# Optimization experiments

Measured on AMD Instinct MI355X. Metric: run time of the kernel, lower is better.

## Reference

```python
import jax, jax.numpy as jnp
import numpy as np

B, PLEN, QLEN, D = 16, 1024, 256, 256
MASK_VALUE = -10000000.0


def setup_inputs() -> dict:
    key = jax.random.key(0)
    k1, k2, k3 = jax.random.split(key, 3)
    passage = jax.random.normal(k1, (B, PLEN, D), dtype=jnp.float32)
    question = jax.random.normal(k2, (B, QLEN, D), dtype=jnp.float32)
    passage_mask = (jnp.arange(PLEN)[None, :] >= int(PLEN * 0.9)).astype(jnp.int32)
    passage_mask = jnp.broadcast_to(passage_mask, (B, PLEN))
    question_mask = (jnp.arange(QLEN)[None, :] >= int(QLEN * 0.9)).astype(jnp.int32)
    question_mask = jnp.broadcast_to(question_mask, (B, QLEN))
    # score_linear: Linear(3d, 1) -> weight vector [3d], scalar bias
    W = jax.random.normal(k3, (3 * D,), dtype=jnp.float32) * 0.05
    b = jnp.zeros((1,), dtype=jnp.float32)
    return {"passage": passage, "question": question,
            "passage_mask": passage_mask, "question_mask": question_mask,
            "W": W, "b": b}


def reference(passage, question, passage_mask, question_mask, W, b):
    d = passage.shape[-1]
    # Decompose Linear([p, q, p*q]) @ W + b into three additive terms --
    # identical math to concat+linear, no [b,plen,qlen,3d] intermediate.
    w_p, w_q, w_pq = W[:d], W[d:2 * d], W[2 * d:]
    score = (jnp.einsum('bpd,d->bp', passage, w_p)[:, :, None]
             + jnp.einsum('bqd,d->bq', question, w_q)[:, None, :]
             + jnp.einsum('bpd,bqd->bpq', passage * w_pq, question)
             + b[0])  # [b, plen, qlen]
    pm = passage_mask.astype(score.dtype)
    qm = question_mask.astype(score.dtype)
    keep = (1.0 - pm)[:, :, None] * (1.0 - qm)[:, None, :]  # [b,plen,qlen]
    mask = 1.0 - keep
    score = score * keep + mask * MASK_VALUE
    p2q_weights = jax.nn.softmax(score, axis=2)
    q2p_weights = jax.nn.softmax(jnp.transpose(score, (0, 2, 1)), axis=2)
    p2q_weights = p2q_weights * keep
    q2p_weights = q2p_weights * jnp.transpose(keep, (0, 2, 1))
    p2q_attention = jnp.einsum('bpq,bqd->bpd', p2q_weights, question)
    q2p_attention = jnp.einsum('bqp,bpd->bqd', q2p_weights, passage)
    coattention = jnp.einsum('bpq,bqd->bpd', p2q_weights, q2p_attention)
    return (p2q_attention, coattention)
```

## Files before the change

kernel.cpp:

```cpp
#include <hip/hip_runtime.h>
#include <math.h>

#define NB 16
#define PLEN 1024
#define QLEN 256
#define DIM 256
#define MASKV -10000000.0f

typedef __attribute__((ext_vector_type(8))) short short8;
typedef __attribute__((ext_vector_type(4))) float f32x4;

union u4x16 { unsigned short u[4]; int2 v; };
union u8x16 { unsigned short u[8]; int4 v; };
union u16x16 { unsigned short u[16]; int4 v[2]; };

__device__ inline unsigned short f2bf(float x) {
  unsigned int u = __float_as_uint(x);
  u += 0x7FFF + ((u >> 16) & 1);
  return (unsigned short)(u >> 16);
}
__device__ inline float bf2f(unsigned short u) {
  return __uint_as_float(((unsigned int)u) << 16);
}
__device__ inline int4 pack8(float4 a, float4 b) {
  u8x16 o;
  o.u[0] = f2bf(a.x); o.u[1] = f2bf(a.y); o.u[2] = f2bf(a.z); o.u[3] = f2bf(a.w);
  o.u[4] = f2bf(b.x); o.u[5] = f2bf(b.y); o.u[6] = f2bf(b.z); o.u[7] = f2bf(b.w);
  return o.v;
}

__global__ __launch_bounds__(1024) void k_scoreA(
    const float* __restrict__ passage, const float* __restrict__ question,
    const float* __restrict__ Wg,
    const int* __restrict__ pmask, const int* __restrict__ qmask,
    const float* __restrict__ bias,
    unsigned short* __restrict__ PbT, unsigned short* __restrict__ QbT,
    float* __restrict__ CL, float* __restrict__ RS,
    unsigned short* __restrict__ P2Q, unsigned short* __restrict__ P2Qt) {
  int bid0 = blockIdx.x;
  int bid = (bid0 & 7) * 32 + (bid0 >> 3);
  int b = bid >> 4;
  int tile = bid & 15;
  int p0 = tile * 64;
  int t = threadIdx.x, lane = t & 63, wv = t >> 6;
  int s = wv >> 2, h = wv & 3;
  __shared__ __align__(16) unsigned short As[2][64][40];
  __shared__ __align__(16) unsigned short Bs[2][256][40];
  __shared__ __align__(16) unsigned short Pl[64][264];
  __shared__ float redL[4][256];
  __shared__ float rowL[64][4];
  __shared__ float spS[64];
  __shared__ float sqS[256];

  int rb = t >> 2, cb = (t & 3) * 8;
  int pr = t >> 4, pc = (t & 15) * 2;
  const float* psrc = passage + ((size_t)b * PLEN + p0 + pr) * DIM;
  const float* qsrc = question + ((size_t)b * QLEN + rb) * DIM;
  const float* wq = Wg + DIM;

  f32x4 acc[4] = {};
  float spp = 0.f, sqq = 0.f;
  float4 qa = *(const float4*)&qsrc[cb];
  float4 qb_ = *(const float4*)&qsrc[cb + 4];
  float2 xv = *(const float2*)(psrc + pc);
  {
    sqq += qa.x * wq[cb]     + qa.y * wq[cb + 1] + qa.z * wq[cb + 2] + qa.w * wq[cb + 3]
         + qb_.x * wq[cb + 4] + qb_.y * wq[cb + 5] + qb_.z * wq[cb + 6] + qb_.w * wq[cb + 7];
    *(int4*)&Bs[0][rb][cb] = pack8(qa, qb_);
    spp += xv.x * Wg[pc] + xv.y * Wg[pc + 1];
    unsigned int raw = (unsigned int)f2bf(xv.x) | (((unsigned int)f2bf(xv.y)) << 16);
    unsigned int wgt = (unsigned int)f2bf(xv.x * Wg[2 * DIM + pc])
                     | (((unsigned int)f2bf(xv.y * Wg[2 * DIM + pc + 1])) << 16);
    *(unsigned int*)&Pl[pr][pc] = raw;
    *(unsigned int*)&As[0][pr][pc] = wgt;
  }
  __syncthreads();
  int cur = 0;
  for (int ki = 0; ki < 8; ++ki) {
    float2 xn; float4 qa2, qb2;
    if (ki < 7) {
      int kt = (ki + 1) * 32;
      qa2 = *(const float4*)&qsrc[kt + cb];
      qb2 = *(const float4*)&qsrc[kt + cb + 4];
      xn = *(const float2*)(psrc + kt + pc);
    }
    short8 af = *(const short8*)&As[cur][s * 16 + (lane & 15)][(lane >> 4) * 8];
    for (int j = 0; j < 4; ++j) {
      short8 bf = *(const short8*)&Bs[cur][h * 64 + j * 16 + (lane & 15)][(lane >> 4) * 8];
      acc[j] = __builtin_amdgcn_mfma_f32_16x16x32_bf16(af, bf, acc[j], 0, 0, 0);
    }
    if (ki < 7) {
      int kt = (ki + 1) * 32;
      int dq = kt + cb, dp = kt + pc;
      sqq += qa2.x * wq[dq]     + qa2.y * wq[dq + 1] + qa2.z * wq[dq + 2] + qa2.w * wq[dq + 3]
           + qb2.x * wq[dq + 4] + qb2.y * wq[dq + 5] + qb2.z * wq[dq + 6] + qb2.w * wq[dq + 7];
      spp += xn.x * Wg[dp] + xn.y * Wg[dp + 1];
      unsigned int raw = (unsigned int)f2bf(xn.x) | (((unsigned int)f2bf(xn.y)) << 16);
      unsigned int wgt = (unsigned int)f2bf(xn.x * Wg[2 * DIM + dp])
                       | (((unsigned int)f2bf(xn.y * Wg[2 * DIM + dp + 1])) << 16);
      int nxt = cur ^ 1;
      *(unsigned int*)&Pl[pr][dp] = raw;
      *(unsigned int*)&As[nxt][pr][pc] = wgt;
      *(int4*)&Bs[nxt][rb][cb] = pack8(qa2, qb2);
      cur = nxt;
    }
    __syncthreads();
  }

  sqq += __shfl_xor(sqq, 1, 64);
  sqq += __shfl_xor(sqq, 2, 64);
  if ((t & 3) == 0) sqS[rb] = sqq;
  spp += __shfl_xor(spp, 1, 64);
  spp += __shfl_xor(spp, 2, 64);
  spp += __shfl_xor(spp, 4, 64);
  spp += __shfl_xor(spp, 8, 64);
  if ((t & 15) == 0) spS[pr] = spp;
  {
    int d = t >> 2, ch = t & 3;
    u16x16 o;
    for (int e = 0; e < 16; ++e) o.u[e] = Pl[ch * 16 + e][d];
    unsigned short* dst = PbT + ((size_t)b * DIM + d) * PLEN + p0 + ch * 16;
    *(int4*)dst = o.v[0];
    *(int4*)(dst + 8) = o.v[1];
  }
  __syncthreads();

  float b0 = bias[0];
  float spv[4]; int pmv[4];
  for (int r = 0; r < 4; ++r) {
    int rl = s * 16 + (lane >> 4) * 4 + r;
    spv[r] = spS[rl] + b0;
    pmv[r] = pmask[b * PLEN + p0 + rl];
  }
  float sqv[4]; int qmv[4];
  for (int j = 0; j < 4; ++j) {
    int q = h * 64 + j * 16 + (lane & 15);
    sqv[j] = sqS[q];
    qmv[j] = qmask[b * QLEN + q];
  }
  for (int j = 0; j < 4; ++j)
    for (int r = 0; r < 4; ++r) {
      float v = acc[j][r] + spv[r] + sqv[j];
      acc[j][r] = (pmv[r] | qmv[j]) ? 0.0f : __expf(v);
    }

  for (int j = 0; j < 4; ++j) {
    float e = acc[j][0] + acc[j][1] + acc[j][2] + acc[j][3];
    e += __shfl_xor(e, 16, 64);
    e += __shfl_xor(e, 32, 64);
    if ((lane >> 4) == 0)
      redL[s][h * 64 + j * 16 + (lane & 15)] = e;
  }
  for (int r = 0; r < 4; ++r) {
    int rl = s * 16 + (lane >> 4) * 4 + r;
    float l = acc[0][r] + acc[1][r] + acc[2][r] + acc[3][r];
    for (int msk = 1; msk <= 8; msk <<= 1) l += __shfl_xor(l, msk, 64);
    if ((lane & 15) == 0) rowL[rl][h] = l;
  }
  __syncthreads();

  if (t < 256) {
    int q = t;
    CL[((size_t)b * 16 + tile) * QLEN + q] = redL[0][q] + redL[1][q] + redL[2][q] + redL[3][q];
  }

  for (int r = 0; r < 4; ++r) {
    int rl = s * 16 + (lane >> 4) * 4 + r;
    float l = rowL[rl][0] + rowL[rl][1] + rowL[rl][2] + rowL[rl][3];
    if (h == 0 && (lane & 15) == 0)
      RS[(size_t)b * PLEN + p0 + rl] = l;
    float inv = (l > 0.f) ? 1.0f / l : 0.0f;
    for (int j = 0; j < 4; ++j)
      Pl[rl][h * 64 + j * 16 + (lane & 15)] = f2bf(acc[j][r] * inv);
  }
  __syncthreads();

  for (int k = 0; k < 2; ++k) {
    int idx = t + k * 1024;
    int row = idx >> 5, c8 = idx & 31;
    *(int4*)&P2Q[((size_t)b * PLEN + p0 + row) * QLEN + c8 * 8] = *(const int4*)&Pl[row][c8 * 8];
  }
  {
    int q = t >> 2, pcc = t & 3;
    u16x16 o;
    for (int e = 0; e < 16; ++e) o.u[e] = Pl[pcc * 16 + e][q];
    unsigned short* dst = P2Qt + ((size_t)b * QLEN + q) * PLEN + p0 + pcc * 16;
    *(int4*)dst = o.v[0];
    *(int4*)(dst + 8) = o.v[1];
  }

  if (tile < 4) {
    __syncthreads();
    int r0 = tile * 64;
    const float* src = question + ((size_t)b * QLEN + r0) * DIM;
    int row = t >> 4, c0 = (t & 15) * 16;
    for (int i = 0; i < 4; ++i) {
      int d = c0 + i * 4;
      float4 x = *(const float4*)&src[(size_t)row * DIM + d];
      u4x16 tv;
      tv.u[0] = f2bf(x.x); tv.u[1] = f2bf(x.y); tv.u[2] = f2bf(x.z); tv.u[3] = f2bf(x.w);
      *(int2*)&Pl[row][d] = tv.v;
    }
    __syncthreads();
    for (int it = 0; it < 2; ++it) {
      int g = t + it * 1024;
      int d = g >> 3, ch = g & 7;
      u8x16 o;
      for (int e = 0; e < 8; ++e) o.u[e] = Pl[ch * 8 + e][d];
      *(int4*)&QbT[(size_t)(b * DIM + d) * QLEN + r0 + ch * 8] = o.v;
    }
  }
}

__global__ __launch_bounds__(512) void k_mid(
    const unsigned short* __restrict__ P2Qt, const unsigned short* __restrict__ PbT,
    const unsigned short* __restrict__ P2Q, const unsigned short* __restrict__ QbT,
    const float* __restrict__ RS, const float* __restrict__ CL,
    unsigned short* __restrict__ QATTt, float* __restrict__ out1) {
  __shared__ __align__(16) char smem[40960];
  int t = threadIdx.x, lane = t & 63, wid = t >> 6;

  if (blockIdx.x < NB * 16) {
    int bid = blockIdx.x;
    int b = bid >> 4, dt = (bid >> 2) & 3, qt = bid & 3;
    int wm = wid >> 2, wn = wid & 3;
    typedef unsigned short row72[72];
    row72* Wt = (row72*)smem;
    row72* At = (row72*)(smem + 18432);
    float* CSs = (float*)(smem + 36864);
    if (t < 64) {
      int q = qt * 64 + t;
      float L = 0.f;
      for (int tm = 0; tm < 16; ++tm)
        L += CL[((size_t)b * 16 + tm) * QLEN + q];
      CSs[t] = (L > 0.f) ? 1.0f / L : 0.0f;
    }

    int rrow = t >> 3;
    int pch = (t & 7) * 8;
    const unsigned short* Wsrc = P2Qt + ((size_t)b * QLEN + qt * 64 + rrow) * PLEN + pch;
    const unsigned short* Asrc = PbT + ((size_t)b * DIM + dt * 64 + rrow) * PLEN + pch;
    const float* rsB = RS + (size_t)b * PLEN + pch;

    f32x4 acc[2] = {};
    int4 wvv = *(const int4*)Wsrc;
    int4 av = *(const int4*)Asrc;
    float4 rs0 = *(const float4*)rsB, rs1 = *(const float4*)(rsB + 4);
    __syncthreads();
    float cs = CSs[rrow];

    {
      float rsv[8] = {rs0.x, rs0.y, rs0.z, rs0.w, rs1.x, rs1.y, rs1.z, rs1.w};
      const unsigned short* wu = (const unsigned short*)&wvv;
      u8x16 wo;
#pragma unroll
      for (int e = 0; e < 8; ++e) wo.u[e] = f2bf(bf2f(wu[e]) * rsv[e] * cs);
      *(int4*)&Wt[rrow][pch] = wo.v;
      *(int4*)&At[rrow][pch] = av;
    }
    __syncthreads();
    int cur = 0;
    for (int ps = 0; ps < 16; ++ps) {
      if (ps < 15) {
        int off = (ps + 1) * 64;
        wvv = *(const int4*)(Wsrc + off);
        av = *(const int4*)(Asrc + off);
        rs0 = *(const float4*)(rsB + off); rs1 = *(const float4*)(rsB + off + 4);
      }
      for (int kk = 0; kk < 64; kk += 32) {
        short8 bf = *(const short8*)&Wt[cur * 64 + wn * 16 + (lane & 15)][kk + (lane >> 4) * 8];
        for (int i = 0; i < 2; ++i) {
          short8 af = *(const short8*)&At[cur * 64 + wm * 32 + i * 16 + (lane & 15)][kk + (lane >> 4) * 8];
          acc[i] = __builtin_amdgcn_mfma_f32_16x16x32_bf16(af, bf, acc[i], 0, 0, 0);
        }
      }
      if (ps < 15) {
        float rsv[8] = {rs0.x, rs0.y, rs0.z, rs0.w, rs1.x, rs1.y, rs1.z, rs1.w};
        const unsigned short* wu = (const unsigned short*)&wvv;
        u8x16 wo;
#pragma unroll
        for (int e = 0; e < 8; ++e) wo.u[e] = f2bf(bf2f(wu[e]) * rsv[e] * cs);
        int nxt = cur ^ 1;
        *(int4*)&Wt[nxt * 64 + rrow][pch] = wo.v;
        *(int4*)&At[nxt * 64 + rrow][pch] = av;
        cur = nxt;
      }
      __syncthreads();
    }
    int d0 = dt * 64 + wm * 32, q0 = qt * 64 + wn * 16;
    for (int i = 0; i < 2; ++i)
      for (int rr = 0; rr < 4; ++rr) {
        int d = d0 + i * 16 + (lane >> 4) * 4 + rr;
        QATTt[((size_t)b * DIM + d) * QLEN + q0 + (lane & 15)] = f2bf(acc[i][rr]);
      }
  } else {
    int u = blockIdx.x - NB * 16;
    int b = u >> 5, tm = (u >> 1) & 15, tn = u & 1;
    const unsigned short* A  = P2Q + ((size_t)b * PLEN + tm * 64) * QLEN;
    const unsigned short* B1 = QbT + ((size_t)b * DIM + tn * 128) * QLEN;
    typedef unsigned short row40[40];
    row40* As2 = (row40*)smem;
    row40* Bq = (row40*)(smem + 10240);
    int wm = wid >> 2, wn = wid & 3;
    f32x4 acc1[2][2] = {};
    int r = t >> 2, c = (t & 3) * 8;
    int4 rb1 = *(const int4*)&B1[(size_t)r * QLEN + c];
    int4 rav;
    if (t < 256) rav = *(const int4*)&A[(size_t)r * QLEN + c];
    *(int4*)&Bq[r][c] = rb1;
    if (t < 256) *(int4*)&As2[r][c] = rav;
    __syncthreads();
    int cur = 0;
    for (int ki = 0; ki < 8; ++ki) {
      if (ki < 7) {
        int kt = (ki + 1) * 32;
        rb1 = *(const int4*)&B1[(size_t)r * QLEN + kt + c];
        if (t < 256) rav = *(const int4*)&A[(size_t)r * QLEN + kt + c];
      }
      short8 af[2], b1v[2];
      for (int i = 0; i < 2; ++i)
        af[i] = *(const short8*)&As2[cur * 64 + wm * 32 + i * 16 + (lane & 15)][(lane >> 4) * 8];
      for (int j = 0; j < 2; ++j)
        b1v[j] = *(const short8*)&Bq[cur * 128 + wn * 32 + j * 16 + (lane & 15)][(lane >> 4) * 8];
      for (int i = 0; i < 2; ++i)
        for (int j = 0; j < 2; ++j)
          acc1[i][j] = __builtin_amdgcn_mfma_f32_16x16x32_bf16(af[i], b1v[j], acc1[i][j], 0, 0, 0);
      if (ki < 7) {
        int nxt = cur ^ 1;
        *(int4*)&Bq[nxt * 128 + r][c] = rb1;
        if (t < 256) *(int4*)&As2[nxt * 64 + r][c] = rav;
        cur = nxt;
      }
      __syncthreads();
    }
    int p0 = tm * 64 + wm * 32, d0 = tn * 128 + wn * 32;
    for (int i = 0; i < 2; ++i)
      for (int rr = 0; rr < 4; ++rr) {
        int p = p0 + i * 16 + (lane >> 4) * 4 + rr;
        size_t rowo = ((size_t)b * PLEN + p) * DIM;
        for (int j = 0; j < 2; ++j) {
          int d = d0 + j * 16 + (lane & 15);
          out1[rowo + d] = acc1[i][j][rr];
        }
      }
  }
}

__global__ __launch_bounds__(512) void k_final2(
    const unsigned short* __restrict__ P2Q, const unsigned short* __restrict__ QATTt,
    float* __restrict__ out2) {
  int bid = blockIdx.x;
  int b = bid >> 5, tm = (bid >> 1) & 15, tn = bid & 1;
  const unsigned short* A  = P2Q + ((size_t)b * PLEN + tm * 64) * QLEN;
  const unsigned short* B2 = QATTt + ((size_t)b * DIM + tn * 128) * QLEN;
  __shared__ __align__(16) unsigned short As[2][64][40];
  __shared__ __align__(16) unsigned short Bc[2][128][40];
  int t = threadIdx.x, lane = t & 63, wid = t >> 6;
  int wm = wid >> 2, wn = wid & 3;
  f32x4 acc[2][2] = {};
  int r = t >> 2, c = (t & 3) * 8;
  int4 rb2 = *(const int4*)&B2[(size_t)r * QLEN + c];
  int4 rav;
  if (t < 256) rav = *(const int4*)&A[(size_t)r * QLEN + c];
  *(int4*)&Bc[0][r][c] = rb2;
  if (t < 256) *(int4*)&As[0][r][c] = rav;
  __syncthreads();
  int cur = 0;
  for (int ki = 0; ki < 8; ++ki) {
    if (ki < 7) {
      int kt = (ki + 1) * 32;
      rb2 = *(const int4*)&B2[(size_t)r * QLEN + kt + c];
      if (t < 256) rav = *(const int4*)&A[(size_t)r * QLEN + kt + c];
    }
    short8 af[2], bc[2];
    for (int i = 0; i < 2; ++i)
      af[i] = *(const short8*)&As[cur][wm * 32 + i * 16 + (lane & 15)][(lane >> 4) * 8];
    for (int j = 0; j < 2; ++j)
      bc[j] = *(const short8*)&Bc[cur][wn * 32 + j * 16 + (lane & 15)][(lane >> 4) * 8];
    for (int i = 0; i < 2; ++i)
      for (int j = 0; j < 2; ++j)
        acc[i][j] = __builtin_amdgcn_mfma_f32_16x16x32_bf16(af[i], bc[j], acc[i][j], 0, 0, 0);
    if (ki < 7) {
      int nxt = cur ^ 1;
      *(int4*)&Bc[nxt][r][c] = rb2;
      if (t < 256) *(int4*)&As[nxt][r][c] = rav;
      cur = nxt;
    }
    __syncthreads();
  }
  int p0 = tm * 64 + wm * 32, d0 = tn * 128 + wn * 32;
  for (int i = 0; i < 2; ++i)
    for (int rr = 0; rr < 4; ++rr) {
      int p = p0 + i * 16 + (lane >> 4) * 4 + rr;
      size_t rowo = ((size_t)b * PLEN + p) * DIM;
      for (int j = 0; j < 2; ++j) {
        int d = d0 + j * 16 + (lane & 15);
        out2[rowo + d] = acc[i][j][rr];
      }
    }
}

extern "C" void kernel_launch(void* const* d_in, const int* in_sizes, int n_in,
                              void* d_out, int out_size, void* d_ws, size_t ws_size,
                              hipStream_t stream) {
  const float* passage  = (const float*)d_in[0];
  const float* question = (const float*)d_in[1];
  const int*   pmask    = (const int*)d_in[2];
  const int*   qmask    = (const int*)d_in[3];
  const float* W        = (const float*)d_in[4];
  const float* bias     = (const float*)d_in[5];
  float* out = (float*)d_out;

  const size_t NS = (size_t)NB * PLEN * QLEN;
  const size_t NQ = (size_t)NB * QLEN * DIM;
  char* w = (char*)d_ws;
  unsigned short* PbT  = (unsigned short*)w; w += NS * 2;
  unsigned short* QbT  = (unsigned short*)w; w += NQ * 2;
  unsigned short* P2Q  = (unsigned short*)w; w += NS * 2;
  unsigned short* P2Qt = (unsigned short*)w; w += NS * 2;
  unsigned short* QATTt = (unsigned short*)w; w += NQ * 2;
  float* CL = (float*)w;                     w += (size_t)NB * 16 * QLEN * 4;
  float* RS = (float*)w;

  float* out1 = out;
  float* out2 = out + (size_t)NB * PLEN * DIM;

  k_scoreA<<<dim3(NB * 16), dim3(1024), 0, stream>>>(
      passage, question, W, pmask, qmask, bias, PbT, QbT, CL, RS, P2Q, P2Qt);
  k_mid<<<dim3(NB * 48), dim3(512), 0, stream>>>(
      P2Qt, PbT, P2Q, QbT, RS, CL, QATTt, out1);
  k_final2<<<dim3(NB * 32), dim3(512), 0, stream>>>(
      P2Q, QATTt, out2);
}
```

Measured before the change: 53.58 us.

## Split score kernel over query halves and defer row normalization to consumers

The score kernel now launches 512 blocks of 512 threads, each covering a 64x128 score tile instead of 64x256, which doubles the grid and shrinks LDS use so more blocks can be resident. The blocks store unnormalized exponentials plus per-half row sums. The 1/rowsum scaling moves into the epilogues of the p2q and coattention GEMMs, which drops the per-element rowsum multiply in k_mid's q2p weighting. The passage bf16 transpose is reassigned to the qh==0 blocks. The cost is some extra stored partial sums and redundant inverse computation in the downstream kernels.

Result: faster. 51.99 us (-3.0%).

```diff
diff --git a/kernel.cpp b/kernel.cpp
--- a/kernel.cpp
+++ b/kernel.cpp
@@ -29,64 +29,80 @@
   return o.v;
 }
 
-__global__ __launch_bounds__(1024) void k_scoreA(
+typedef unsigned short row40[40];
+typedef unsigned short row136[136];
+typedef unsigned short row264[264];
+
+#define SM_AS   0
+#define SM_BS   10240
+#define SM_REDL 30720
+#define SM_ROWL 32768
+#define SM_SPS  33280
+#define SM_SQS  33536
+#define SM_PL   34048
+#define SM_TOT  51456
+
+__global__ __launch_bounds__(512, 4) void k_scoreA(
     const float* __restrict__ passage, const float* __restrict__ question,
     const float* __restrict__ Wg,
     const int* __restrict__ pmask, const int* __restrict__ qmask,
     const float* __restrict__ bias,
     unsigned short* __restrict__ PbT, unsigned short* __restrict__ QbT,
-    float* __restrict__ CL, float* __restrict__ RS,
-    unsigned short* __restrict__ P2Q, unsigned short* __restrict__ P2Qt) {
+    float* __restrict__ CL, float* __restrict__ RS2,
+    unsigned short* __restrict__ E, unsigned short* __restrict__ Et) {
+  __shared__ __align__(16) char smem[SM_TOT];
+  row40* As = (row40*)(smem + SM_AS);
+  row40* Bs = (row40*)(smem + SM_BS);
+  float (*redL)[128] = (float(*)[128])(smem + SM_REDL);
+  float (*rowL)[2] = (float(*)[2])(smem + SM_ROWL);
+  float* spS = (float*)(smem + SM_SPS);
+  float* sqS = (float*)(smem + SM_SQS);
+  row136* Pl = (row136*)(smem + SM_PL);
+
   int bid0 = blockIdx.x;
-  int bid = (bid0 & 7) * 32 + (bid0 >> 3);
-  int b = bid >> 4;
-  int tile = bid & 15;
-  int p0 = tile * 64;
+  int bid = (bid0 & 7) * 64 + (bid0 >> 3);
+  int b = bid >> 5;
+  int tile = (bid >> 1) & 15;
+  int qh = bid & 1;
+  int p0 = tile * 64, q0 = qh * 128;
   int t = threadIdx.x, lane = t & 63, wv = t >> 6;
-  int s = wv >> 2, h = wv & 3;
-  __shared__ __align__(16) unsigned short As[2][64][40];
-  __shared__ __align__(16) unsigned short Bs[2][256][40];
-  __shared__ __align__(16) unsigned short Pl[64][264];
-  __shared__ float redL[4][256];
-  __shared__ float rowL[64][4];
-  __shared__ float spS[64];
-  __shared__ float sqS[256];
+  int s = wv >> 1, h = wv & 1;
 
   int rb = t >> 2, cb = (t & 3) * 8;
-  int pr = t >> 4, pc = (t & 15) * 2;
+  int pr = t >> 3, pc = (t & 7) * 4;
   const float* psrc = passage + ((size_t)b * PLEN + p0 + pr) * DIM;
-  const float* qsrc = question + ((size_t)b * QLEN + rb) * DIM;
+  const float* qsrc = question + ((size_t)b * QLEN + q0 + rb) * DIM;
   const float* wq = Wg + DIM;
+  const float* wpq = Wg + 2 * DIM;
 
   f32x4 acc[4] = {};
   float spp = 0.f, sqq = 0.f;
-  float4 qa = *(const float4*)&qsrc[cb];
-  float4 qb_ = *(const float4*)&qsrc[cb + 4];
-  float2 xv = *(const float2*)(psrc + pc);
   {
+    float4 qa = *(const float4*)&qsrc[cb];
+    float4 qb_ = *(const float4*)&qsrc[cb + 4];
+    float4 x = *(const float4*)&psrc[pc];
     sqq += qa.x * wq[cb]     + qa.y * wq[cb + 1] + qa.z * wq[cb + 2] + qa.w * wq[cb + 3]
          + qb_.x * wq[cb + 4] + qb_.y * wq[cb + 5] + qb_.z * wq[cb + 6] + qb_.w * wq[cb + 7];
-    *(int4*)&Bs[0][rb][cb] = pack8(qa, qb_);
-    spp += xv.x * Wg[pc] + xv.y * Wg[pc + 1];
-    unsigned int raw = (unsigned int)f2bf(xv.x) | (((unsigned int)f2bf(xv.y)) << 16);
-    unsigned int wgt = (unsigned int)f2bf(xv.x * Wg[2 * DIM + pc])
-                     | (((unsigned int)f2bf(xv.y * Wg[2 * DIM + pc + 1])) << 16);
-    *(unsigned int*)&Pl[pr][pc] = raw;
-    *(unsigned int*)&As[0][pr][pc] = wgt;
+    spp += x.x * Wg[pc] + x.y * Wg[pc + 1] + x.z * Wg[pc + 2] + x.w * Wg[pc + 3];
+    *(int4*)&Bs[0 * 128 + rb][cb] = pack8(qa, qb_);
+    u4x16 wg4;
+    wg4.u[0] = f2bf(x.x * wpq[pc]);     wg4.u[1] = f2bf(x.y * wpq[pc + 1]);
+    wg4.u[2] = f2bf(x.z * wpq[pc + 2]); wg4.u[3] = f2bf(x.w * wpq[pc + 3]);
+    *(int2*)&As[0 * 64 + pr][pc] = wg4.v;
   }
   __syncthreads();
   int cur = 0;
   for (int ki = 0; ki < 8; ++ki) {
-    float2 xn; float4 qa2, qb2;
+    float4 qa2, qb2, xn;
     if (ki < 7) {
       int kt = (ki + 1) * 32;
       qa2 = *(const float4*)&qsrc[kt + cb];
       qb2 = *(const float4*)&qsrc[kt + cb + 4];
-      xn = *(const float2*)(psrc + kt + pc);
-    }
-    short8 af = *(const short8*)&As[cur][s * 16 + (lane & 15)][(lane >> 4) * 8];
+      xn = *(const float4*)&psrc[kt + pc];
+    }
+    short8 af = *(const short8*)&As[cur * 64 + s * 16 + (lane & 15)][(lane >> 4) * 8];
     for (int j = 0; j < 4; ++j) {
-      short8 bf = *(const short8*)&Bs[cur][h * 64 + j * 16 + (lane & 15)][(lane >> 4) * 8];
+      short8 bf = *(const short8*)&Bs[cur * 128 + h * 64 + j * 16 + (lane & 15)][(lane >> 4) * 8];
       acc[j] = __builtin_amdgcn_mfma_f32_16x16x32_bf16(af, bf, acc[j], 0, 0, 0);
     }
     if (ki < 7) {
@@ -94,14 +110,13 @@
       int dq = kt + cb, dp = kt + pc;
       sqq += qa2.x * wq[dq]     + qa2.y * wq[dq + 1] + qa2.z * wq[dq + 2] + qa2.w * wq[dq + 3]
            + qb2.x * wq[dq + 4] + qb2.y * wq[dq + 5] + qb2.z * wq[dq + 6] + qb2.w * wq[dq + 7];
-      spp += xn.x * Wg[dp] + xn.y * Wg[dp + 1];
-      unsigned int raw = (unsigned int)f2bf(xn.x) | (((unsigned int)f2bf(xn.y)) << 16);
-      unsigned int wgt = (unsigned int)f2bf(xn.x * Wg[2 * DIM + dp])
-                       | (((unsigned int)f2bf(xn.y * Wg[2 * DIM + dp + 1])) << 16);
+      spp += xn.x * Wg[dp] + xn.y * Wg[dp + 1] + xn.z * Wg[dp + 2] + xn.w * Wg[dp + 3];
       int nxt = cur ^ 1;
-      *(unsigned int*)&Pl[pr][dp] = raw;
-      *(unsigned int*)&As[nxt][pr][pc] = wgt;
-      *(int4*)&Bs[nxt][rb][cb] = pack8(qa2, qb2);
+      *(int4*)&Bs[nxt * 128 + rb][cb] = pack8(qa2, qb2);
+      u4x16 wg4;
+      wg4.u[0] = f2bf(xn.x * wpq[dp]);     wg4.u[1] = f2bf(xn.y * wpq[dp + 1]);
+      wg4.u[2] = f2bf(xn.z * wpq[dp + 2]); wg4.u[3] = f2bf(xn.w * wpq[dp + 3]);
+      *(int2*)&As[nxt * 64 + pr][pc] = wg4.v;
       cur = nxt;
     }
     __syncthreads();
@@ -113,16 +128,7 @@
   spp += __shfl_xor(spp, 1, 64);
   spp += __shfl_xor(spp, 2, 64);
   spp += __shfl_xor(spp, 4, 64);
-  spp += __shfl_xor(spp, 8, 64);
-  if ((t & 15) == 0) spS[pr] = spp;
-  {
-    int d = t >> 2, ch = t & 3;
-    u16x16 o;
-    for (int e = 0; e < 16; ++e) o.u[e] = Pl[ch * 16 + e][d];
-    unsigned short* dst = PbT + ((size_t)b * DIM + d) * PLEN + p0 + ch * 16;
-    *(int4*)dst = o.v[0];
-    *(int4*)(dst + 8) = o.v[1];
-  }
+  if ((t & 7) == 0) spS[pr] = spp;
   __syncthreads();
 
   float b0 = bias[0];
@@ -134,16 +140,15 @@
   }
   float sqv[4]; int qmv[4];
   for (int j = 0; j < 4; ++j) {
-    int q = h * 64 + j * 16 + (lane & 15);
-    sqv[j] = sqS[q];
-    qmv[j] = qmask[b * QLEN + q];
+    int ql = h * 64 + j * 16 + (lane & 15);
+    sqv[j] = sqS[ql];
+    qmv[j] = qmask[b * QLEN + q0 + ql];
   }
   for (int j = 0; j < 4; ++j)
     for (int r = 0; r < 4; ++r) {
       float v = acc[j][r] + spv[r] + sqv[j];
       acc[j][r] = (pmv[r] | qmv[j]) ? 0.0f : __expf(v);
     }
-
   for (int j = 0; j < 4; ++j) {
     float e = acc[j][0] + acc[j][1] + acc[j][2] + acc[j][3];
     e += __shfl_xor(e, 16, 64);
@@ -157,65 +162,80 @@
     for (int msk = 1; msk <= 8; msk <<= 1) l += __shfl_xor(l, msk, 64);
     if ((lane & 15) == 0) rowL[rl][h] = l;
   }
-  __syncthreads();
-
-  if (t < 256) {
-    int q = t;
-    CL[((size_t)b * 16 + tile) * QLEN + q] = redL[0][q] + redL[1][q] + redL[2][q] + redL[3][q];
-  }
-
   for (int r = 0; r < 4; ++r) {
     int rl = s * 16 + (lane >> 4) * 4 + r;
-    float l = rowL[rl][0] + rowL[rl][1] + rowL[rl][2] + rowL[rl][3];
-    if (h == 0 && (lane & 15) == 0)
-      RS[(size_t)b * PLEN + p0 + rl] = l;
-    float inv = (l > 0.f) ? 1.0f / l : 0.0f;
     for (int j = 0; j < 4; ++j)
-      Pl[rl][h * 64 + j * 16 + (lane & 15)] = f2bf(acc[j][r] * inv);
+      Pl[rl][h * 64 + j * 16 + (lane & 15)] = f2bf(acc[j][r]);
   }
   __syncthreads();
 
+  if (t < 128) {
+    CL[((size_t)b * 16 + tile) * QLEN + q0 + t] = redL[0][t] + redL[1][t] + redL[2][t] + redL[3][t];
+  } else if (t < 192) {
+    int rl = t - 128;
+    RS2[((size_t)b * PLEN + p0 + rl) * 2 + qh] = rowL[rl][0] + rowL[rl][1];
+  }
+
   for (int k = 0; k < 2; ++k) {
-    int idx = t + k * 1024;
-    int row = idx >> 5, c8 = idx & 31;
-    *(int4*)&P2Q[((size_t)b * PLEN + p0 + row) * QLEN + c8 * 8] = *(const int4*)&Pl[row][c8 * 8];
+    int idx = t + k * 512;
+    int row = idx >> 4, c8 = idx & 15;
+    *(int4*)&E[((size_t)b * PLEN + p0 + row) * QLEN + q0 + c8 * 8] = *(const int4*)&Pl[row][c8 * 8];
   }
   {
-    int q = t >> 2, pcc = t & 3;
+    int ql = t >> 2, pcc = t & 3;
     u16x16 o;
-    for (int e = 0; e < 16; ++e) o.u[e] = Pl[pcc * 16 + e][q];
-    unsigned short* dst = P2Qt + ((size_t)b * QLEN + q) * PLEN + p0 + pcc * 16;
+    for (int e = 0; e < 16; ++e) o.u[e] = Pl[pcc * 16 + e][ql];
+    unsigned short* dst = Et + ((size_t)b * QLEN + q0 + ql) * PLEN + p0 + pcc * 16;
     *(int4*)dst = o.v[0];
     *(int4*)(dst + 8) = o.v[1];
   }
-
-  if (tile < 4) {
-    __syncthreads();
-    int r0 = tile * 64;
-    const float* src = question + ((size_t)b * QLEN + r0) * DIM;
-    int row = t >> 4, c0 = (t & 15) * 16;
-    for (int i = 0; i < 4; ++i) {
+  __syncthreads();
+
+  row264* TT = (row264*)smem;
+  if (qh == 0) {
+    const float* src = passage + ((size_t)b * PLEN + p0) * DIM;
+    int row = t >> 3, c0 = (t & 7) * 32;
+    for (int i = 0; i < 8; ++i) {
       int d = c0 + i * 4;
       float4 x = *(const float4*)&src[(size_t)row * DIM + d];
       u4x16 tv;
       tv.u[0] = f2bf(x.x); tv.u[1] = f2bf(x.y); tv.u[2] = f2bf(x.z); tv.u[3] = f2bf(x.w);
-      *(int2*)&Pl[row][d] = tv.v;
-    }
-    __syncthreads();
-    for (int it = 0; it < 2; ++it) {
-      int g = t + it * 1024;
-      int d = g >> 3, ch = g & 7;
+      *(int2*)&TT[row][d] = tv.v;
+    }
+    __syncthreads();
+    for (int it = 0; it < 4; ++it) {
+      int g = t + it * 512;
+      int dd = g >> 3, ch = g & 7;
       u8x16 o;
-      for (int e = 0; e < 8; ++e) o.u[e] = Pl[ch * 8 + e][d];
-      *(int4*)&QbT[(size_t)(b * DIM + d) * QLEN + r0 + ch * 8] = o.v;
+      for (int e = 0; e < 8; ++e) o.u[e] = TT[ch * 8 + e][dd];
+      *(int4*)&PbT[((size_t)b * DIM + dd) * PLEN + p0 + ch * 8] = o.v;
+    }
+  } else if (tile < 4) {
+    int r0 = tile * 64;
+    const float* src = question + ((size_t)b * QLEN + r0) * DIM;
+    int row = t >> 3, c0 = (t & 7) * 32;
+    for (int i = 0; i < 8; ++i) {
+      int d = c0 + i * 4;
+      float4 x = *(const float4*)&src[(size_t)row * DIM + d];
+      u4x16 tv;
+      tv.u[0] = f2bf(x.x); tv.u[1] = f2bf(x.y); tv.u[2] = f2bf(x.z); tv.u[3] = f2bf(x.w);
+      *(int2*)&TT[row][d] = tv.v;
+    }
+    __syncthreads();
+    for (int it = 0; it < 4; ++it) {
+      int g = t + it * 512;
+      int dd = g >> 3, ch = g & 7;
+      u8x16 o;
+      for (int e = 0; e < 8; ++e) o.u[e] = TT[ch * 8 + e][dd];
+      *(int4*)&QbT[((size_t)b * DIM + dd) * QLEN + r0 + ch * 8] = o.v;
     }
   }
 }
 
 __global__ __launch_bounds__(512) void k_mid(
-    const unsigned short* __restrict__ P2Qt, const unsigned short* __restrict__ PbT,
-    const unsigned short* __restrict__ P2Q, const unsigned short* __restrict__ QbT,
-    const float* __restrict__ RS, const float* __restrict__ CL,
+    const unsigned short* __restrict__ Et, const unsigned short* __restrict__ PbT,
+    const unsigned short* __restrict__ E, const unsigned short* __restrict__ QbT,
+    const float* __restrict__ RS2, const float* __restrict__ CL,
     unsigned short* __restrict__ QATTt, float* __restrict__ out1) {
   __shared__ __align__(16) char smem[40960];
   int t = threadIdx.x, lane = t & 63, wid = t >> 6;
@@ -238,23 +258,20 @@
 
     int rrow = t >> 3;
     int pch = (t & 7) * 8;
-    const unsigned short* Wsrc = P2Qt + ((size_t)b * QLEN + qt * 64 + rrow) * PLEN + pch;
+    const unsigned short* Wsrc = Et + ((size_t)b * QLEN + qt * 64 + rrow) * PLEN + pch;
     const unsigned short* Asrc = PbT + ((size_t)b * DIM + dt * 64 + rrow) * PLEN + pch;
-    const float* rsB = RS + (size_t)b * PLEN + pch;
 
     f32x4 acc[2] = {};
     int4 wvv = *(const int4*)Wsrc;
     int4 av = *(const int4*)Asrc;
-    float4 rs0 = *(const float4*)rsB, rs1 = *(const float4*)(rsB + 4);
     __syncthreads();
     float cs = CSs[rrow];
 
     {
-      float rsv[8] = {rs0.x, rs0.y, rs0.z, rs0.w, rs1.x, rs1.y, rs1.z, rs1.w};
       const unsigned short* wu = (const unsigned short*)&wvv;
       u8x16 wo;
 #pragma unroll
-      for (int e = 0; e < 8; ++e) wo.u[e] = f2bf(bf2f(wu[e]) * rsv[e] * cs);
+      for (int e = 0; e < 8; ++e) wo.u[e] = f2bf(bf2f(wu[e]) * cs);
       *(int4*)&Wt[rrow][pch] = wo.v;
       *(int4*)&At[rrow][pch] = av;
     }
@@ -265,7 +282,6 @@
         int off = (ps + 1) * 64;
         wvv = *(const int4*)(Wsrc + off);
         av = *(const int4*)(Asrc + off);
-        rs0 = *(const float4*)(rsB + off); rs1 = *(const float4*)(rsB + off + 4);
       }
       for (int kk = 0; kk < 64; kk += 32) {
         short8 bf = *(const short8*)&Wt[cur * 64 + wn * 16 + (lane & 15)][kk + (lane >> 4) * 8];
@@ -275,11 +291,10 @@
         }
       }
       if (ps < 15) {
-        float rsv[8] = {rs0.x, rs0.y, rs0.z, rs0.w, rs1.x, rs1.y, rs1.z, rs1.w};
         const unsigned short* wu = (const unsigned short*)&wvv;
         u8x16 wo;
 #pragma unroll
-        for (int e = 0; e < 8; ++e) wo.u[e] = f2bf(bf2f(wu[e]) * rsv[e] * cs);
+        for (int e = 0; e < 8; ++e) wo.u[e] = f2bf(bf2f(wu[e]) * cs);
         int nxt = cur ^ 1;
         *(int4*)&Wt[nxt * 64 + rrow][pch] = wo.v;
         *(int4*)&At[nxt * 64 + rrow][pch] = av;
@@ -296,12 +311,18 @@
   } else {
     int u = blockIdx.x - NB * 16;
     int b = u >> 5, tm = (u >> 1) & 15, tn = u & 1;
-    const unsigned short* A  = P2Q + ((size_t)b * PLEN + tm * 64) * QLEN;
+    const unsigned short* A  = E + ((size_t)b * PLEN + tm * 64) * QLEN;
     const unsigned short* B1 = QbT + ((size_t)b * DIM + tn * 128) * QLEN;
-    typedef unsigned short row40[40];
-    row40* As2 = (row40*)smem;
-    row40* Bq = (row40*)(smem + 10240);
+    typedef unsigned short row40k[40];
+    row40k* As2 = (row40k*)smem;
+    row40k* Bq = (row40k*)(smem + 10240);
+    float* invS = (float*)(smem + 30720);
     int wm = wid >> 2, wn = wid & 3;
+    if (t < 64) {
+      float rs = RS2[((size_t)b * PLEN + tm * 64 + t) * 2]
+               + RS2[((size_t)b * PLEN + tm * 64 + t) * 2 + 1];
+      invS[t] = (rs > 0.f) ? 1.0f / rs : 0.0f;
+    }
     f32x4 acc1[2][2] = {};
     int r = t >> 2, c = (t & 3) * 8;
     int4 rb1 = *(const int4*)&B1[(size_t)r * QLEN + c];
@@ -336,27 +357,35 @@
     int p0 = tm * 64 + wm * 32, d0 = tn * 128 + wn * 32;
     for (int i = 0; i < 2; ++i)
       for (int rr = 0; rr < 4; ++rr) {
-        int p = p0 + i * 16 + (lane >> 4) * 4 + rr;
+        int pl = wm * 32 + i * 16 + (lane >> 4) * 4 + rr;
+        float inv = invS[pl];
+        int p = tm * 64 + pl;
         size_t rowo = ((size_t)b * PLEN + p) * DIM;
         for (int j = 0; j < 2; ++j) {
           int d = d0 + j * 16 + (lane & 15);
-          out1[rowo + d] = acc1[i][j][rr];
+          out1[rowo + d] = acc1[i][j][rr] * inv;
         }
       }
   }
 }
 
 __global__ __launch_bounds__(512) void k_final2(
-    const unsigned short* __restrict__ P2Q, const unsigned short* __restrict__ QATTt,
-    float* __restrict__ out2) {
+    const unsigned short* __restrict__ E, const unsigned short* __restrict__ QATTt,
+    const float* __restrict__ RS2, float* __restrict__ out2) {
   int bid = blockIdx.x;
   int b = bid >> 5, tm = (bid >> 1) & 15, tn = bid & 1;
-  const unsigned short* A  = P2Q + ((size_t)b * PLEN + tm * 64) * QLEN;
+  const unsigned short* A  = E + ((size_t)b * PLEN + tm * 64) * QLEN;
   const unsigned short* B2 = QATTt + ((size_t)b * DIM + tn * 128) * QLEN;
   __shared__ __align__(16) unsigned short As[2][64][40];
   __shared__ __align__(16) unsigned short Bc[2][128][40];
+  __shared__ float invS[64];
   int t = threadIdx.x, lane = t & 63, wid = t >> 6;
   int wm = wid >> 2, wn = wid & 3;
+  if (t < 64) {
+    float rs = RS2[((size_t)b * PLEN + tm * 64 + t) * 2]
+             + RS2[((size_t)b * PLEN + tm * 64 + t) * 2 + 1];
+    invS[t] = (rs > 0.f) ? 1.0f / rs : 0.0f;
+  }
   f32x4 acc[2][2] = {};
   int r = t >> 2, c = (t & 3) * 8;
   int4 rb2 = *(const int4*)&B2[(size_t)r * QLEN + c];
@@ -388,14 +417,16 @@
     }
     __syncthreads();
   }
-  int p0 = tm * 64 + wm * 32, d0 = tn * 128 + wn * 32;
+  int d0 = tn * 128 + wn * 32;
   for (int i = 0; i < 2; ++i)
     for (int rr = 0; rr < 4; ++rr) {
-      int p = p0 + i * 16 + (lane >> 4) * 4 + rr;
+      int pl = wm * 32 + i * 16 + (lane >> 4) * 4 + rr;
+      float inv = invS[pl];
+      int p = tm * 64 + pl;
       size_t rowo = ((size_t)b * PLEN + p) * DIM;
       for (int j = 0; j < 2; ++j) {
         int d = d0 + j * 16 + (lane & 15);
-        out2[rowo + d] = acc[i][j][rr];
+        out2[rowo + d] = acc[i][j][rr] * inv;
       }
     }
 }
@@ -416,19 +447,19 @@
   char* w = (char*)d_ws;
   unsigned short* PbT  = (unsigned short*)w; w += NS * 2;
   unsigned short* QbT  = (unsigned short*)w; w += NQ * 2;
-  unsigned short* P2Q  = (unsigned short*)w; w += NS * 2;
-  unsigned short* P2Qt = (unsigned short*)w; w += NS * 2;
+  unsigned short* E    = (unsigned short*)w; w += NS * 2;
+  unsigned short* Et   = (unsigned short*)w; w += NS * 2;
   unsigned short* QATTt = (unsigned short*)w; w += NQ * 2;
-  float* CL = (float*)w;                     w += (size_t)NB * 16 * QLEN * 4;
-  float* RS = (float*)w;
+  float* CL  = (float*)w;                    w += (size_t)NB * 16 * QLEN * 4;
+  float* RS2 = (float*)w;
 
   float* out1 = out;
   float* out2 = out + (size_t)NB * PLEN * DIM;
 
-  k_scoreA<<<dim3(NB * 16), dim3(1024), 0, stream>>>(
-      passage, question, W, pmask, qmask, bias, PbT, QbT, CL, RS, P2Q, P2Qt);
+  k_scoreA<<<dim3(512), dim3(512), 0, stream>>>(
+      passage, question, W, pmask, qmask, bias, PbT, QbT, CL, RS2, E, Et);
   k_mid<<<dim3(NB * 48), dim3(512), 0, stream>>>(
-      P2Qt, PbT, P2Q, QbT, RS, CL, QATTt, out1);
+      Et, PbT, E, QbT, RS2, CL, QATTt, out1);
   k_final2<<<dim3(NB * 32), dim3(512), 0, stream>>>(
-      P2Q, QATTt, out2);
-}
+      E, QATTt, RS2, out2);
+}
```
